# Kernel tuning notes

Hardware: AMD Instinct MI355X
Metric: run time of the kernel (lower is better)

The kernel has to match this reference:

```python
import jax, jax.numpy as jnp
import numpy as np

# Static multi-scale pyramid metadata (spatial_shapes / level_start_index in torch)
SHAPES = [(92, 160), (46, 80), (23, 40), (12, 20)]
B, NQ, C, NH, DH, L, P, DFF = 2, 10000, 256, 8, 32, 4, 4, 1024
S = sum(h * w for h, w in SHAPES)


def layer_norm(x, g, b, eps=1e-5):
    m = x.mean(-1, keepdims=True)
    v = ((x - m) ** 2).mean(-1, keepdims=True)
    return (x - m) * jax.lax.rsqrt(v + eps) * g + b


def ms_deform(value, loc, attn):
    """Multi-scale deformable attention core (grid_sample bilinear, zero padding).
    value: [B,S,NH,DH], loc: [B,NQ,NH,L,P,2] normalized (x,y), attn: [B,NQ,NH,L,P]."""
    out = jnp.zeros((B, NH, NQ, DH), value.dtype)
    start = 0
    for lvl, (Hh, Ww) in enumerate(SHAPES):
        v = value[:, start:start + Hh * Ww].transpose(0, 2, 1, 3)  # [B,NH,HW,DH]
        start += Hh * Ww
        l = loc[:, :, :, lvl].transpose(0, 2, 1, 3, 4)             # [B,NH,NQ,P,2]
        # align_corners=False pixel coords
        x = l[..., 0] * Ww - 0.5
        y = l[..., 1] * Hh - 0.5
        x0 = jnp.floor(x); y0 = jnp.floor(y)
        lx = x - x0; ly = y - y0
        x0i = x0.astype(jnp.int32); y0i = y0.astype(jnp.int32)
        samp = jnp.zeros((B, NH, NQ, P, DH), value.dtype)
        for dx, dy, w in ((0, 0, (1 - lx) * (1 - ly)), (1, 0, lx * (1 - ly)),
                          (0, 1, (1 - lx) * ly), (1, 1, lx * ly)):
            xi = x0i + dx; yi = y0i + dy
            valid = (xi >= 0) & (xi < Ww) & (yi >= 0) & (yi < Hh)
            idx = (jnp.clip(yi, 0, Hh - 1) * Ww + jnp.clip(xi, 0, Ww - 1)).reshape(B, NH, NQ * P)
            g = jnp.take_along_axis(v, jnp.broadcast_to(idx[..., None], (B, NH, NQ * P, DH)), axis=2)
            samp = samp + g.reshape(B, NH, NQ, P, DH) * (w * valid)[..., None]
        out = out + jnp.einsum('bhnpd,bhnp->bhnd', samp, attn[:, :, :, lvl].transpose(0, 2, 1, 3))
    return out.transpose(0, 2, 1, 3).reshape(B, NQ, NH * DH)


def setup_inputs() -> dict:
    ks = jax.random.split(jax.random.key(0), 12)
    sc = C ** -0.5
    return {
        'src': jax.random.normal(ks[0], (B, S, C), jnp.float32),
        'q_feat': jax.random.normal(ks[1], (B, NQ, C), jnp.float32),
        'q_pos': jax.random.normal(ks[2], (B, NQ, C), jnp.float32) * 0.1,
        'q_ref': jax.random.uniform(ks[3], (B, NQ, 2), jnp.float32),
        'valid_ratios': jnp.ones((B, L, 2), jnp.float32),
        'Wv': jax.random.normal(ks[4], (C, C), jnp.float32) * sc,
        'bv': jnp.zeros((C,), jnp.float32),
        'Woff': jax.random.normal(ks[5], (C, NH * L * P * 2), jnp.float32) * 0.01,
        'boff': jax.random.uniform(ks[6], (NH * L * P * 2,), jnp.float32, minval=-0.5, maxval=0.5),
        'Wa': jax.random.normal(ks[7], (C, NH * L * P), jnp.float32) * sc,
        'ba': jnp.zeros((NH * L * P,), jnp.float32),
        'Wo': jax.random.normal(ks[8], (C, C), jnp.float32) * sc,
        'bo': jnp.zeros((C,), jnp.float32),
        'g1': jnp.ones((C,), jnp.float32), 'be1': jnp.zeros((C,), jnp.float32),
        'W1': jax.random.normal(ks[9], (C, DFF), jnp.float32) * sc,
        'bf1': jnp.zeros((DFF,), jnp.float32),
        'W2': jax.random.normal(ks[10], (DFF, C), jnp.float32) * (DFF ** -0.5),
        'bf2': jnp.zeros((C,), jnp.float32),
        'g2': jnp.ones((C,), jnp.float32), 'be2': jnp.zeros((C,), jnp.float32),
    }


def reference(src, q_feat, q_pos, q_ref, valid_ratios, Wv, bv, Woff, boff, Wa, ba,
              Wo, bo, g1, be1, W1, bf1, W2, bf2, g2, be2):
    # reference_points = q_reference_points[:,:,None] * valid_ratios[:,None]
    ref = q_ref[:, :, None, :] * valid_ratios[:, None]          # [B,NQ,L,2]
    # MSDeformAttn
    value = (src @ Wv + bv).reshape(B, S, NH, DH)
    q = q_feat + q_pos
    off = (q @ Woff + boff).reshape(B, NQ, NH, L, P, 2)
    attn = jax.nn.softmax((q @ Wa + ba).reshape(B, NQ, NH, L * P), axis=-1).reshape(B, NQ, NH, L, P)
    normalizer = jnp.array([[w, h] for h, w in SHAPES], src.dtype)  # [L,2] (W,H)
    loc = ref[:, :, None, :, None, :] + off / normalizer[None, None, None, :, None, :]
    a = ms_deform(value, loc, attn) @ Wo + bo
    # residual + LN + FFN (dropout is identity at inference)
    x = layer_norm(q_feat + a, g1, be1)
    ffn = jax.nn.relu(x @ W1 + bf1) @ W2 + bf2
    return layer_norm(x + ffn, g2, be2)
```

## Files before the change

kernel.cpp:

```cpp
#include <hip/hip_runtime.h>
#include <hip/hip_bf16.h>
#include <cstdint>

#define B_   2
#define NQ_  10000
#define C_   256
#define NH_  8
#define DH_  32
#define DFF_ 1024
#define S_   19560
#define MQ_P 20096
#define MV_P 39168

typedef __attribute__((ext_vector_type(8))) short short8;
typedef __attribute__((ext_vector_type(4))) float f32x4;

__device__ __forceinline__ void gload16(const void* g, void* l) {
  __builtin_amdgcn_global_load_lds(
      (const __attribute__((address_space(1))) unsigned int*)g,
      (__attribute__((address_space(3))) unsigned int*)l, 16, 0, 0);
}

__device__ __forceinline__ float bflo(unsigned u) {
  union { unsigned u; float f; } c; c.u = u << 16; return c.f;
}
__device__ __forceinline__ float bfhi(unsigned u) {
  union { unsigned u; float f; } c; c.u = u & 0xffff0000u; return c.f;
}

__global__ __launch_bounds__(256) void conv_weights(
    const float* __restrict__ Wv, const float* __restrict__ Woff,
    const float* __restrict__ Wa, const float* __restrict__ Wo,
    const float* __restrict__ W1, const float* __restrict__ W2,
    __hip_bfloat16* __restrict__ wbase) {
  __shared__ float tile[64][65];
  int blk = blockIdx.x;
  const float* W; __hip_bfloat16* Wt; int K, N;
  if (blk < 16)       { W = Wv;   Wt = wbase + 0;      K = 256;  N = 256; }
  else if (blk < 32)  { W = Woff; Wt = wbase + 65536;  K = 256;  N = 256;  blk -= 16; }
  else if (blk < 40)  { W = Wa;   Wt = wbase + 131072; K = 256;  N = 128;  blk -= 32; }
  else if (blk < 56)  { W = Wo;   Wt = wbase + 163840; K = 256;  N = 256;  blk -= 40; }
  else if (blk < 120) { W = W1;   Wt = wbase + 229376; K = 256;  N = 1024; blk -= 56; }
  else                { W = W2;   Wt = wbase + 491520; K = 1024; N = 256;  blk -= 120; }
  const int ntiles = N >> 6;
  const int kt = blk / ntiles, nt = blk % ntiles;
  const int c = threadIdx.x & 63, r0 = threadIdx.x >> 6;
#pragma unroll
  for (int i = 0; i < 16; ++i) {
    const int r = r0 + i * 4;
    tile[r][c] = W[(long)(kt * 64 + r) * N + nt * 64 + c];
  }
  __syncthreads();
#pragma unroll
  for (int i = 0; i < 16; ++i) {
    const int n = r0 + i * 4;
    Wt[(long)(nt * 64 + n) * K + kt * 64 + c] = __float2bfloat16(tile[c][n]);
  }
}

__global__ __launch_bounds__(256) void prep_q(
    const float* __restrict__ qf, const float* __restrict__ qp,
    __hip_bfloat16* __restrict__ q_bf) {
  long idx = (long)blockIdx.x * 256 + threadIdx.x;
  int row = idx >> 5, c8 = (idx & 31) * 8;
  union { __hip_bfloat16 h[8]; uint4 u; } o;
  if (row < B_ * NQ_) {
    const float4 a0 = *reinterpret_cast<const float4*>(qf + (long)row * 256 + c8);
    const float4 a1 = *reinterpret_cast<const float4*>(qf + (long)row * 256 + c8 + 4);
    const float4 b0 = *reinterpret_cast<const float4*>(qp + (long)row * 256 + c8);
    const float4 b1 = *reinterpret_cast<const float4*>(qp + (long)row * 256 + c8 + 4);
    o.h[0] = __float2bfloat16(a0.x + b0.x); o.h[1] = __float2bfloat16(a0.y + b0.y);
    o.h[2] = __float2bfloat16(a0.z + b0.z); o.h[3] = __float2bfloat16(a0.w + b0.w);
    o.h[4] = __float2bfloat16(a1.x + b1.x); o.h[5] = __float2bfloat16(a1.y + b1.y);
    o.h[6] = __float2bfloat16(a1.z + b1.z); o.h[7] = __float2bfloat16(a1.w + b1.w);
  } else o.u = make_uint4(0, 0, 0, 0);
  *reinterpret_cast<uint4*>(q_bf + (long)row * 256 + c8) = o.u;
}

template <int MODE>
__global__ __launch_bounds__(256) void gemm_bf16(
    const __hip_bfloat16* __restrict__ A, const __hip_bfloat16* __restrict__ Bt,
    const float* __restrict__ bias, const float* __restrict__ bias2, int bsplit,
    void* __restrict__ Cp, int M, int N, int K) {
  __shared__ short smA[64 * 64];
  __shared__ short smB[128 * 64];
  const int tid = threadIdx.x;
  const int lane = tid & 63;
  const int w = tid >> 6;
  const int wr = w >> 1, wc = w & 1;
  const long bm = (long)blockIdx.x * 64;
  const long bn = (long)blockIdx.y * 128;

  f32x4 acc[2][4];
#pragma unroll
  for (int i = 0; i < 2; ++i)
#pragma unroll
    for (int j = 0; j < 4; ++j) acc[i][j] = (f32x4)(0.f);

  const int srow = tid >> 3;
  const int su = (tid & 7) ^ (srow & 7);
  const __hip_bfloat16* Ag = A + (bm + srow) * (long)K + su * 8;
  const __hip_bfloat16* Bg = Bt + (bn + srow) * (long)K + su * 8;
  char* lA = (char*)smA + tid * 16;
  char* lB = (char*)smB + tid * 16;

  for (int k0 = 0; k0 < K; k0 += 64) {
    gload16(Ag,           lA);
    gload16(Ag + 32L * K, lA + 4096);
    gload16(Bg,           lB);
    gload16(Bg + 32L * K, lB + 4096);
    gload16(Bg + 64L * K, lB + 8192);
    gload16(Bg + 96L * K, lB + 12288);
    Ag += 64; Bg += 64;
    __syncthreads();
#pragma unroll
    for (int ks = 0; ks < 2; ++ks) {
      const int u = ks * 4 + (lane >> 4);
      short8 af[2], bf[4];
#pragma unroll
      for (int mi = 0; mi < 2; ++mi) {
        const int r = wr * 32 + (lane & 15) + mi * 16;
        af[mi] = *reinterpret_cast<const short8*>(
            (char*)smA + r * 128 + ((u ^ (r & 7)) * 16));
      }
#pragma unroll
      for (int ni = 0; ni < 4; ++ni) {
        const int r = wc * 64 + (lane & 15) + ni * 16;
        bf[ni] = *reinterpret_cast<const short8*>(
            (char*)smB + r * 128 + ((u ^ (r & 7)) * 16));
      }
#pragma unroll
      for (int mi = 0; mi < 2; ++mi)
#pragma unroll
        for (int ni = 0; ni < 4; ++ni)
          acc[mi][ni] = __builtin_amdgcn_mfma_f32_16x16x32_bf16(af[mi], bf[ni], acc[mi][ni], 0, 0, 0);
    }
    __syncthreads();
  }

  const int crow0 = wr * 32 + ((lane >> 4) << 2);
  const int ccol0 = wc * 64 + (lane & 15);
#pragma unroll
  for (int mi = 0; mi < 2; ++mi) {
#pragma unroll
    for (int ni = 0; ni < 4; ++ni) {
      const int col = bn + ccol0 + ni * 16;
      const float bs = (col < bsplit) ? bias[col] : bias2[col - bsplit];
#pragma unroll
      for (int r = 0; r < 4; ++r) {
        const long row = bm + crow0 + mi * 16 + r;
        float v = acc[mi][ni][r] + bs;
        if (MODE == 0) {
          ((float*)Cp)[row * N + col] = v;
        } else if (MODE == 2) {
          ((__hip_bfloat16*)Cp)[row * N + col] = __float2bfloat16(fmaxf(v, 0.f));
        } else {
          ((__hip_bfloat16*)Cp)[row * N + col] = __float2bfloat16(v);
        }
      }
    }
  }
}

__global__ __launch_bounds__(256) void gemm_val(
    const float* __restrict__ A, const __hip_bfloat16* __restrict__ Bt,
    const float* __restrict__ bias, __hip_bfloat16* __restrict__ Cp, int Mreal) {
  __shared__ short smA[64 * 64];
  __shared__ short smB[256 * 64];
  const int tid = threadIdx.x;
  const int lane = tid & 63;
  const int w = tid >> 6;
  const long bm = (long)blockIdx.x * 64;

  f32x4 acc[4][4];
#pragma unroll
  for (int i = 0; i < 4; ++i)
#pragma unroll
    for (int j = 0; j < 4; ++j) acc[i][j] = (f32x4)(0.f);

  const int ar = tid >> 2;
  const int au = (tid & 3) * 2;
  const bool arow_ok = (bm + ar) < Mreal;
  const float* Afp = A + (bm + ar) * 256L + au * 8;
  char* wA0 = (char*)smA + ar * 128 + ((au ^ (ar & 7)) * 16);
  char* wA1 = (char*)smA + ar * 128 + (((au + 1) ^ (ar & 7)) * 16);

  const int srow = tid >> 3;
  const int su = (tid & 7) ^ (srow & 7);
  const __hip_bfloat16* Bg = Bt + (long)srow * 256 + su * 8;
  char* lB = (char*)smB + tid * 16;

  for (int k0 = 0; k0 < 256; k0 += 64) {
#pragma unroll
    for (int j = 0; j < 8; ++j) gload16(Bg + 32L * j * 256, lB + 4096 * j);
    Bg += 64;
    float4 f0 = make_float4(0.f, 0.f, 0.f, 0.f), f1 = f0, f2 = f0, f3 = f0;
    if (arow_ok) {
      f0 = *reinterpret_cast<const float4*>(Afp + k0);
      f1 = *reinterpret_cast<const float4*>(Afp + k0 + 4);
      f2 = *reinterpret_cast<const float4*>(Afp + k0 + 8);
      f3 = *reinterpret_cast<const float4*>(Afp + k0 + 12);
    }
    union { __hip_bfloat16 h[8]; uint4 u; } c0, c1;
    c0.h[0] = __float2bfloat16(f0.x); c0.h[1] = __float2bfloat16(f0.y);
    c0.h[2] = __float2bfloat16(f0.z); c0.h[3] = __float2bfloat16(f0.w);
    c0.h[4] = __float2bfloat16(f1.x); c0.h[5] = __float2bfloat16(f1.y);
    c0.h[6] = __float2bfloat16(f1.z); c0.h[7] = __float2bfloat16(f1.w);
    c1.h[0] = __float2bfloat16(f2.x); c1.h[1] = __float2bfloat16(f2.y);
    c1.h[2] = __float2bfloat16(f2.z); c1.h[3] = __float2bfloat16(f2.w);
    c1.h[4] = __float2bfloat16(f3.x); c1.h[5] = __float2bfloat16(f3.y);
    c1.h[6] = __float2bfloat16(f3.z); c1.h[7] = __float2bfloat16(f3.w);
    *reinterpret_cast<uint4*>(wA0) = c0.u;
    *reinterpret_cast<uint4*>(wA1) = c1.u;
    __syncthreads();
#pragma unroll
    for (int ks = 0; ks < 2; ++ks) {
      const int u = ks * 4 + (lane >> 4);
      short8 af[4], bf[4];
#pragma unroll
      for (int mi = 0; mi < 4; ++mi) {
        const int r = (lane & 15) + mi * 16;
        af[mi] = *reinterpret_cast<const short8*>(
            (char*)smA + r * 128 + ((u ^ (r & 7)) * 16));
      }
#pragma unroll
      for (int ni = 0; ni < 4; ++ni) {
        const int r = w * 64 + ni * 16 + (lane & 15);
        bf[ni] = *reinterpret_cast<const short8*>(
            (char*)smB + r * 128 + ((u ^ (r & 7)) * 16));
      }
#pragma unroll
      for (int mi = 0; mi < 4; ++mi)
#pragma unroll
        for (int ni = 0; ni < 4; ++ni)
          acc[mi][ni] = __builtin_amdgcn_mfma_f32_16x16x32_bf16(af[mi], bf[ni], acc[mi][ni], 0, 0, 0);
    }
    __syncthreads();
  }

  const int crow0 = (lane >> 4) << 2;
  const int cl = lane & 15;
#pragma unroll
  for (int mi = 0; mi < 4; ++mi) {
#pragma unroll
    for (int ni = 0; ni < 4; ++ni) {
      const int col = w * 64 + ni * 16 + cl;
      const float bs = bias[col];
      const int h = col >> 5, dh = col & 31;
#pragma unroll
      for (int r = 0; r < 4; ++r) {
        const long row = bm + mi * 16 + crow0 + r;
        if (row < Mreal) {
          const int b = (row >= S_) ? 1 : 0;
          const long s = row - (long)b * S_;
          Cp[(((long)(b * 8 + h)) * S_ + s) * 32 + dh] =
              __float2bfloat16(acc[mi][ni][r] + bs);
        }
      }
    }
  }
}

__global__ __launch_bounds__(256) void msdeform_kernel(
    const __hip_bfloat16* __restrict__ value, const __hip_bfloat16* __restrict__ oa,
    const float* __restrict__ q_ref, const float* __restrict__ vr,
    __hip_bfloat16* __restrict__ out) {
  const int t = blockIdx.x * 256 + threadIdx.x;
  const int tid7 = t & 127;
  const int dq = tid7 & 3;
  const int l = (tid7 >> 2) & 3;
  const int h = tid7 >> 4;
  const int bq = __builtin_amdgcn_readfirstlane(t >> 7);
  const int b = (bq >= NQ_) ? 1 : 0;

  const int W  = (l == 0) ? 160 : (l == 1) ? 80 : (l == 2) ? 40 : 20;
  const int H  = (l == 0) ? 92  : (l == 1) ? 46 : (l == 2) ? 23 : 12;
  const int S0 = (l == 0) ? 0 : (l == 1) ? 14720 : (l == 2) ? 18400 : 19320;

  const __hip_bfloat16* oabase = oa + (long)bq * 384;
  const uint2 mu = *reinterpret_cast<const uint2*>(oabase + 256 + h * 16 + l * 4);
  const float l0 = bflo(mu.x), l1 = bfhi(mu.x), l2 = bflo(mu.y), l3 = bfhi(mu.y);
  float mx = fmaxf(fmaxf(l0, l1), fmaxf(l2, l3));
  mx = fmaxf(mx, __shfl_xor(mx, 4, 64));
  mx = fmaxf(mx, __shfl_xor(mx, 8, 64));
  const float e0 = __expf(l0 - mx), e1 = __expf(l1 - mx);
  const float e2 = __expf(l2 - mx), e3 = __expf(l3 - mx);
  float sum = e0 + e1 + e2 + e3;
  sum += __shfl_xor(sum, 4, 64);
  sum += __shfl_xor(sum, 8, 64);
  const float inv = 1.f / sum;
  const float w0 = e0 * inv, w1 = e1 * inv, w2 = e2 * inv, w3 = e3 * inv;

  const uint4 ou = *reinterpret_cast<const uint4*>(oabase + h * 32 + l * 8);

  const float rx = q_ref[(long)bq * 2 + 0];
  const float ry = q_ref[(long)bq * 2 + 1];
  const float2 vv = *reinterpret_cast<const float2*>(vr + (b * 4 + l) * 2);
  const float refxW = rx * vv.x * W - 0.5f;
  const float refyH = ry * vv.y * H - 0.5f;
  const unsigned base32 = (unsigned)(((b * 8 + h) * S_ + S0) * 32 + dq * 8);

  unsigned offs[16]; float wts[16];
#define COORD(s, OX, OY, AW)                                                   \
  {                                                                            \
    const float x = refxW + (OX);                                              \
    const float y = refyH + (OY);                                              \
    const float x0f = floorf(x), y0f = floorf(y);                              \
    const float lx = x - x0f, ly = y - y0f;                                    \
    const int x0 = (int)x0f, y0 = (int)y0f;                                    \
    const int x1 = x0 + 1, y1 = y0 + 1;                                        \
    const float wx0 = ((unsigned)x0 < (unsigned)W) ? (1.f - lx) : 0.f;         \
    const float wx1 = ((unsigned)x1 < (unsigned)W) ? lx : 0.f;                 \
    const float wy0 = ((unsigned)y0 < (unsigned)H) ? (1.f - ly) : 0.f;         \
    const float wy1 = ((unsigned)y1 < (unsigned)H) ? ly : 0.f;                 \
    const int x0c = min(max(x0, 0), W - 1);                                    \
    const int x1c = min(max(x1, 0), W - 1);                                    \
    const int y0c = min(max(y0, 0), H - 1);                                    \
    const int y1c = min(max(y1, 0), H - 1);                                    \
    const unsigned r0o = base32 + (unsigned)(y0c * W) * 32;                    \
    const unsigned r1o = base32 + (unsigned)(y1c * W) * 32;                    \
    offs[4 * (s) + 0] = r0o + (unsigned)x0c * 32;                              \
    offs[4 * (s) + 1] = r0o + (unsigned)x1c * 32;                              \
    offs[4 * (s) + 2] = r1o + (unsigned)x0c * 32;                              \
    offs[4 * (s) + 3] = r1o + (unsigned)x1c * 32;                              \
    wts[4 * (s) + 0] = (AW) * wx0 * wy0;                                       \
    wts[4 * (s) + 1] = (AW) * wx1 * wy0;                                       \
    wts[4 * (s) + 2] = (AW) * wx0 * wy1;                                       \
    wts[4 * (s) + 3] = (AW) * wx1 * wy1;                                       \
  }
  COORD(0, bflo(ou.x), bfhi(ou.x), w0)
  COORD(1, bflo(ou.y), bfhi(ou.y), w1)
  COORD(2, bflo(ou.z), bfhi(ou.z), w2)
  COORD(3, bflo(ou.w), bfhi(ou.w), w3)
#undef COORD

  uint4 d[16];
#pragma unroll
  for (int j = 0; j < 16; ++j)
    d[j] = *reinterpret_cast<const uint4*>(value + offs[j]);
  __builtin_amdgcn_sched_barrier(0);

  float acc[8] = {};
#pragma unroll
  for (int j = 0; j < 16; ++j) {
    const float ww = wts[j];
    acc[0] += ww * bflo(d[j].x); acc[1] += ww * bfhi(d[j].x);
    acc[2] += ww * bflo(d[j].y); acc[3] += ww * bfhi(d[j].y);
    acc[4] += ww * bflo(d[j].z); acc[5] += ww * bfhi(d[j].z);
    acc[6] += ww * bflo(d[j].w); acc[7] += ww * bfhi(d[j].w);
  }

#pragma unroll
  for (int j = 0; j < 8; ++j) acc[j] += __shfl_xor(acc[j], 4, 64);
#pragma unroll
  for (int j = 0; j < 8; ++j) acc[j] += __shfl_xor(acc[j], 8, 64);

  if (l == 0) {
    union { __hip_bfloat16 hh[8]; uint4 u; } o0;
#pragma unroll
    for (int j = 0; j < 8; ++j) o0.hh[j] = __float2bfloat16(acc[j]);
    *reinterpret_cast<uint4*>(out + (long)bq * 256 + h * 32 + dq * 8) = o0.u;
  }
}

__global__ __launch_bounds__(256) void add_ln_kernel(
    const float* __restrict__ res, const float* __restrict__ xin,
    const float* __restrict__ gamma, const float* __restrict__ beta,
    float* __restrict__ out, __hip_bfloat16* __restrict__ out_bf, int nrows) {
  int row = blockIdx.x * 4 + (threadIdx.x >> 6);
  int lane = threadIdx.x & 63;
  if (row >= nrows) return;
  const float4 r4 = *reinterpret_cast<const float4*>(res + (long)row * 256 + lane * 4);
  const float4 x4 = *reinterpret_cast<const float4*>(xin + (long)row * 256 + lane * 4);
  float tv[4] = {r4.x + x4.x, r4.y + x4.y, r4.z + x4.z, r4.w + x4.w};
  float s = tv[0] + tv[1] + tv[2] + tv[3];
#pragma unroll
  for (int o = 32; o > 0; o >>= 1) s += __shfl_xor(s, o, 64);
  float mean = s * (1.f / 256.f);
  float vs = 0.f;
#pragma unroll
  for (int j = 0; j < 4; ++j) { float dd = tv[j] - mean; vs += dd * dd; }
#pragma unroll
  for (int o = 32; o > 0; o >>= 1) vs += __shfl_xor(vs, o, 64);
  float inv = rsqrtf(vs * (1.f / 256.f) + 1e-5f);
  const float4 g = *reinterpret_cast<const float4*>(gamma + lane * 4);
  const float4 be = *reinterpret_cast<const float4*>(beta + lane * 4);
  float4 o4;
  o4.x = (tv[0] - mean) * inv * g.x + be.x;
  o4.y = (tv[1] - mean) * inv * g.y + be.y;
  o4.z = (tv[2] - mean) * inv * g.z + be.z;
  o4.w = (tv[3] - mean) * inv * g.w + be.w;
  *reinterpret_cast<float4*>(out + (long)row * 256 + lane * 4) = o4;
  if (out_bf) {
    union { __hip_bfloat16 h[4]; uint2 u; } p;
    p.h[0] = __float2bfloat16(o4.x); p.h[1] = __float2bfloat16(o4.y);
    p.h[2] = __float2bfloat16(o4.z); p.h[3] = __float2bfloat16(o4.w);
    *reinterpret_cast<uint2*>(out_bf + (long)row * 256 + lane * 4) = p.u;
  }
}

extern "C" void kernel_launch(void* const* d_in, const int* in_sizes, int n_in,
                              void* d_out, int out_size, void* d_ws, size_t ws_size,
                              hipStream_t stream) {
  const float* src    = (const float*)d_in[0];
  const float* q_feat = (const float*)d_in[1];
  const float* q_pos  = (const float*)d_in[2];
  const float* q_ref  = (const float*)d_in[3];
  const float* vr     = (const float*)d_in[4];
  const float* Wv     = (const float*)d_in[5];
  const float* bv     = (const float*)d_in[6];
  const float* Woff   = (const float*)d_in[7];
  const float* boff   = (const float*)d_in[8];
  const float* Wa     = (const float*)d_in[9];
  const float* ba     = (const float*)d_in[10];
  const float* Wo     = (const float*)d_in[11];
  const float* bo     = (const float*)d_in[12];
  const float* g1     = (const float*)d_in[13];
  const float* be1    = (const float*)d_in[14];
  const float* W1     = (const float*)d_in[15];
  const float* bf1    = (const float*)d_in[16];
  const float* W2     = (const float*)d_in[17];
  const float* bf2    = (const float*)d_in[18];
  const float* g2     = (const float*)d_in[19];
  const float* be2    = (const float*)d_in[20];

  char* ws = (char*)d_ws;
  __hip_bfloat16* val_bf = (__hip_bfloat16*)(ws + 0);
  __hip_bfloat16* q_bf   = (__hip_bfloat16*)(ws + 20029440);
  float*          a_f    = (float*)(ws + 0);
  __hip_bfloat16* h1_bf  = (__hip_bfloat16*)(ws + 0);
  __hip_bfloat16* oa_bf  = (__hip_bfloat16*)(ws + 41156608);
  float*          f2_f   = (float*)(ws + 41156608);
  __hip_bfloat16* ms_bf  = (__hip_bfloat16*)(ws + 61734912);
  float*          x_f    = (float*)(ws + 72024064);
  __hip_bfloat16* x_bf   = (__hip_bfloat16*)(ws + 92602368);
  __hip_bfloat16* wts    = (__hip_bfloat16*)(ws + 102891520);
  float* outp = (float*)d_out;

  const int Mq = B_ * NQ_;
  const int Mv = B_ * S_;
  const int BIG = 1 << 30;

  conv_weights<<<184, 256, 0, stream>>>(Wv, Woff, Wa, Wo, W1, W2, wts);
  prep_q<<<MQ_P * 32 / 256, 256, 0, stream>>>(q_feat, q_pos, q_bf);
  gemm_val<<<MV_P / 64, 256, 0, stream>>>(src, wts + 0, bv, val_bf, Mv);
  gemm_bf16<4><<<dim3(MQ_P / 64, 3), 256, 0, stream>>>(q_bf, wts + 65536, boff, ba, 256, oa_bf, MQ_P, 384, 256);
  msdeform_kernel<<<(Mq * 128) / 256, 256, 0, stream>>>(val_bf, oa_bf, q_ref, vr, ms_bf);
  gemm_bf16<0><<<dim3(MQ_P / 64, 2), 256, 0, stream>>>(ms_bf, wts + 163840, bo, bo, BIG, a_f, MQ_P, 256, 256);
  add_ln_kernel<<<(Mq + 3) / 4, 256, 0, stream>>>(q_feat, a_f, g1, be1, x_f, x_bf, Mq);
  gemm_bf16<2><<<dim3(MQ_P / 64, 8), 256, 0, stream>>>(x_bf, wts + 229376, bf1, bf1, BIG, h1_bf, MQ_P, 1024, 256);
  gemm_bf16<0><<<dim3(MQ_P / 64, 2), 256, 0, stream>>>(h1_bf, wts + 491520, bf2, bf2, BIG, f2_f, MQ_P, 256, 1024);
  add_ln_kernel<<<(Mq + 3) / 4, 256, 0, stream>>>(x_f, f2_f, g2, be2, outp, nullptr, Mq);
}
```

Measured before the change: 167.9 us.

## Store intermediate activations in bf16, merge prep kernels, pack deform accumulation

```diff
diff --git a/kernel.cpp b/kernel.cpp
--- a/kernel.cpp
+++ b/kernel.cpp
@@ -14,6 +14,7 @@
 
 typedef __attribute__((ext_vector_type(8))) short short8;
 typedef __attribute__((ext_vector_type(4))) float f32x4;
+typedef __attribute__((ext_vector_type(2))) float f32x2;
 
 __device__ __forceinline__ void gload16(const void* g, void* l) {
   __builtin_amdgcn_global_load_lds(
@@ -28,53 +29,53 @@
   union { unsigned u; float f; } c; c.u = u & 0xffff0000u; return c.f;
 }
 
-__global__ __launch_bounds__(256) void conv_weights(
+__global__ __launch_bounds__(256) void prep_all(
     const float* __restrict__ Wv, const float* __restrict__ Woff,
     const float* __restrict__ Wa, const float* __restrict__ Wo,
     const float* __restrict__ W1, const float* __restrict__ W2,
-    __hip_bfloat16* __restrict__ wbase) {
-  __shared__ float tile[64][65];
-  int blk = blockIdx.x;
-  const float* W; __hip_bfloat16* Wt; int K, N;
-  if (blk < 16)       { W = Wv;   Wt = wbase + 0;      K = 256;  N = 256; }
-  else if (blk < 32)  { W = Woff; Wt = wbase + 65536;  K = 256;  N = 256;  blk -= 16; }
-  else if (blk < 40)  { W = Wa;   Wt = wbase + 131072; K = 256;  N = 128;  blk -= 32; }
-  else if (blk < 56)  { W = Wo;   Wt = wbase + 163840; K = 256;  N = 256;  blk -= 40; }
-  else if (blk < 120) { W = W1;   Wt = wbase + 229376; K = 256;  N = 1024; blk -= 56; }
-  else                { W = W2;   Wt = wbase + 491520; K = 1024; N = 256;  blk -= 120; }
-  const int ntiles = N >> 6;
-  const int kt = blk / ntiles, nt = blk % ntiles;
-  const int c = threadIdx.x & 63, r0 = threadIdx.x >> 6;
-#pragma unroll
-  for (int i = 0; i < 16; ++i) {
-    const int r = r0 + i * 4;
-    tile[r][c] = W[(long)(kt * 64 + r) * N + nt * 64 + c];
-  }
-  __syncthreads();
-#pragma unroll
-  for (int i = 0; i < 16; ++i) {
-    const int n = r0 + i * 4;
-    Wt[(long)(nt * 64 + n) * K + kt * 64 + c] = __float2bfloat16(tile[c][n]);
-  }
-}
-
-__global__ __launch_bounds__(256) void prep_q(
+    __hip_bfloat16* __restrict__ wbase,
     const float* __restrict__ qf, const float* __restrict__ qp,
     __hip_bfloat16* __restrict__ q_bf) {
-  long idx = (long)blockIdx.x * 256 + threadIdx.x;
-  int row = idx >> 5, c8 = (idx & 31) * 8;
-  union { __hip_bfloat16 h[8]; uint4 u; } o;
-  if (row < B_ * NQ_) {
-    const float4 a0 = *reinterpret_cast<const float4*>(qf + (long)row * 256 + c8);
-    const float4 a1 = *reinterpret_cast<const float4*>(qf + (long)row * 256 + c8 + 4);
-    const float4 b0 = *reinterpret_cast<const float4*>(qp + (long)row * 256 + c8);
-    const float4 b1 = *reinterpret_cast<const float4*>(qp + (long)row * 256 + c8 + 4);
-    o.h[0] = __float2bfloat16(a0.x + b0.x); o.h[1] = __float2bfloat16(a0.y + b0.y);
-    o.h[2] = __float2bfloat16(a0.z + b0.z); o.h[3] = __float2bfloat16(a0.w + b0.w);
-    o.h[4] = __float2bfloat16(a1.x + b1.x); o.h[5] = __float2bfloat16(a1.y + b1.y);
-    o.h[6] = __float2bfloat16(a1.z + b1.z); o.h[7] = __float2bfloat16(a1.w + b1.w);
-  } else o.u = make_uint4(0, 0, 0, 0);
-  *reinterpret_cast<uint4*>(q_bf + (long)row * 256 + c8) = o.u;
+  __shared__ float tile[64][65];
+  if (blockIdx.x < 184) {
+    int blk = blockIdx.x;
+    const float* W; __hip_bfloat16* Wt; int K, N;
+    if (blk < 16)       { W = Wv;   Wt = wbase + 0;      K = 256;  N = 256; }
+    else if (blk < 32)  { W = Woff; Wt = wbase + 65536;  K = 256;  N = 256;  blk -= 16; }
+    else if (blk < 40)  { W = Wa;   Wt = wbase + 131072; K = 256;  N = 128;  blk -= 32; }
+    else if (blk < 56)  { W = Wo;   Wt = wbase + 163840; K = 256;  N = 256;  blk -= 40; }
+    else if (blk < 120) { W = W1;   Wt = wbase + 229376; K = 256;  N = 1024; blk -= 56; }
+    else                { W = W2;   Wt = wbase + 491520; K = 1024; N = 256;  blk -= 120; }
+    const int ntiles = N >> 6;
+    const int kt = blk / ntiles, nt = blk % ntiles;
+    const int c = threadIdx.x & 63, r0 = threadIdx.x >> 6;
+#pragma unroll
+    for (int i = 0; i < 16; ++i) {
+      const int r = r0 + i * 4;
+      tile[r][c] = W[(long)(kt * 64 + r) * N + nt * 64 + c];
+    }
+    __syncthreads();
+#pragma unroll
+    for (int i = 0; i < 16; ++i) {
+      const int n = r0 + i * 4;
+      Wt[(long)(nt * 64 + n) * K + kt * 64 + c] = __float2bfloat16(tile[c][n]);
+    }
+  } else {
+    long idx = (long)(blockIdx.x - 184) * 256 + threadIdx.x;
+    int row = idx >> 5, c8 = (idx & 31) * 8;
+    union { __hip_bfloat16 h[8]; uint4 u; } o;
+    if (row < B_ * NQ_) {
+      const float4 a0 = *reinterpret_cast<const float4*>(qf + (long)row * 256 + c8);
+      const float4 a1 = *reinterpret_cast<const float4*>(qf + (long)row * 256 + c8 + 4);
+      const float4 b0 = *reinterpret_cast<const float4*>(qp + (long)row * 256 + c8);
+      const float4 b1 = *reinterpret_cast<const float4*>(qp + (long)row * 256 + c8 + 4);
+      o.h[0] = __float2bfloat16(a0.x + b0.x); o.h[1] = __float2bfloat16(a0.y + b0.y);
+      o.h[2] = __float2bfloat16(a0.z + b0.z); o.h[3] = __float2bfloat16(a0.w + b0.w);
+      o.h[4] = __float2bfloat16(a1.x + b1.x); o.h[5] = __float2bfloat16(a1.y + b1.y);
+      o.h[6] = __float2bfloat16(a1.z + b1.z); o.h[7] = __float2bfloat16(a1.w + b1.w);
+    } else o.u = make_uint4(0, 0, 0, 0);
+    *reinterpret_cast<uint4*>(q_bf + (long)row * 256 + c8) = o.u;
+  }
 }
 
 template <int MODE>
@@ -150,9 +151,7 @@
       for (int r = 0; r < 4; ++r) {
         const long row = bm + crow0 + mi * 16 + r;
         float v = acc[mi][ni][r] + bs;
-        if (MODE == 0) {
-          ((float*)Cp)[row * N + col] = v;
-        } else if (MODE == 2) {
+        if (MODE == 2) {
           ((__hip_bfloat16*)Cp)[row * N + col] = __float2bfloat16(fmaxf(v, 0.f));
         } else {
           ((__hip_bfloat16*)Cp)[row * N + col] = __float2bfloat16(v);
@@ -340,39 +339,57 @@
     d[j] = *reinterpret_cast<const uint4*>(value + offs[j]);
   __builtin_amdgcn_sched_barrier(0);
 
-  float acc[8] = {};
+  f32x2 acc2[4];
+#pragma unroll
+  for (int i = 0; i < 4; ++i) acc2[i] = (f32x2)(0.f);
 #pragma unroll
   for (int j = 0; j < 16; ++j) {
-    const float ww = wts[j];
-    acc[0] += ww * bflo(d[j].x); acc[1] += ww * bfhi(d[j].x);
-    acc[2] += ww * bflo(d[j].y); acc[3] += ww * bfhi(d[j].y);
-    acc[4] += ww * bflo(d[j].z); acc[5] += ww * bfhi(d[j].z);
-    acc[6] += ww * bflo(d[j].w); acc[7] += ww * bfhi(d[j].w);
-  }
-
-#pragma unroll
-  for (int j = 0; j < 8; ++j) acc[j] += __shfl_xor(acc[j], 4, 64);
-#pragma unroll
-  for (int j = 0; j < 8; ++j) acc[j] += __shfl_xor(acc[j], 8, 64);
+    const f32x2 ww2 = (f32x2)(wts[j]);
+    f32x2 v0, v1, v2, v3;
+    v0.x = bflo(d[j].x); v0.y = bfhi(d[j].x);
+    v1.x = bflo(d[j].y); v1.y = bfhi(d[j].y);
+    v2.x = bflo(d[j].z); v2.y = bfhi(d[j].z);
+    v3.x = bflo(d[j].w); v3.y = bfhi(d[j].w);
+    acc2[0] += ww2 * v0;
+    acc2[1] += ww2 * v1;
+    acc2[2] += ww2 * v2;
+    acc2[3] += ww2 * v3;
+  }
+
+  float accf[8] = {acc2[0].x, acc2[0].y, acc2[1].x, acc2[1].y,
+                   acc2[2].x, acc2[2].y, acc2[3].x, acc2[3].y};
+#pragma unroll
+  for (int j = 0; j < 8; ++j) accf[j] += __shfl_xor(accf[j], 4, 64);
+#pragma unroll
+  for (int j = 0; j < 8; ++j) accf[j] += __shfl_xor(accf[j], 8, 64);
 
   if (l == 0) {
     union { __hip_bfloat16 hh[8]; uint4 u; } o0;
 #pragma unroll
-    for (int j = 0; j < 8; ++j) o0.hh[j] = __float2bfloat16(acc[j]);
+    for (int j = 0; j < 8; ++j) o0.hh[j] = __float2bfloat16(accf[j]);
     *reinterpret_cast<uint4*>(out + (long)bq * 256 + h * 32 + dq * 8) = o0.u;
   }
 }
 
-__global__ __launch_bounds__(256) void add_ln_kernel(
-    const float* __restrict__ res, const float* __restrict__ xin,
+template <bool RES_F32, bool OUT_F32>
+__global__ __launch_bounds__(256) void add_ln2(
+    const void* __restrict__ resv, const __hip_bfloat16* __restrict__ xin,
     const float* __restrict__ gamma, const float* __restrict__ beta,
-    float* __restrict__ out, __hip_bfloat16* __restrict__ out_bf, int nrows) {
+    float* __restrict__ outF, __hip_bfloat16* __restrict__ outB, int nrows) {
   int row = blockIdx.x * 4 + (threadIdx.x >> 6);
   int lane = threadIdx.x & 63;
   if (row >= nrows) return;
-  const float4 r4 = *reinterpret_cast<const float4*>(res + (long)row * 256 + lane * 4);
-  const float4 x4 = *reinterpret_cast<const float4*>(xin + (long)row * 256 + lane * 4);
-  float tv[4] = {r4.x + x4.x, r4.y + x4.y, r4.z + x4.z, r4.w + x4.w};
+  float rv[4];
+  if (RES_F32) {
+    const float4 r4 = *reinterpret_cast<const float4*>((const float*)resv + (long)row * 256 + lane * 4);
+    rv[0] = r4.x; rv[1] = r4.y; rv[2] = r4.z; rv[3] = r4.w;
+  } else {
+    const uint2 r2 = *reinterpret_cast<const uint2*>((const __hip_bfloat16*)resv + (long)row * 256 + lane * 4);
+    rv[0] = bflo(r2.x); rv[1] = bfhi(r2.x); rv[2] = bflo(r2.y); rv[3] = bfhi(r2.y);
+  }
+  const uint2 x2 = *reinterpret_cast<const uint2*>(xin + (long)row * 256 + lane * 4);
+  float tv[4] = {rv[0] + bflo(x2.x), rv[1] + bfhi(x2.x),
+                 rv[2] + bflo(x2.y), rv[3] + bfhi(x2.y)};
   float s = tv[0] + tv[1] + tv[2] + tv[3];
 #pragma unroll
   for (int o = 32; o > 0; o >>= 1) s += __shfl_xor(s, o, 64);
@@ -385,17 +402,19 @@
   float inv = rsqrtf(vs * (1.f / 256.f) + 1e-5f);
   const float4 g = *reinterpret_cast<const float4*>(gamma + lane * 4);
   const float4 be = *reinterpret_cast<const float4*>(beta + lane * 4);
-  float4 o4;
-  o4.x = (tv[0] - mean) * inv * g.x + be.x;
-  o4.y = (tv[1] - mean) * inv * g.y + be.y;
-  o4.z = (tv[2] - mean) * inv * g.z + be.z;
-  o4.w = (tv[3] - mean) * inv * g.w + be.w;
-  *reinterpret_cast<float4*>(out + (long)row * 256 + lane * 4) = o4;
-  if (out_bf) {
+  float o4[4];
+  o4[0] = (tv[0] - mean) * inv * g.x + be.x;
+  o4[1] = (tv[1] - mean) * inv * g.y + be.y;
+  o4[2] = (tv[2] - mean) * inv * g.z + be.z;
+  o4[3] = (tv[3] - mean) * inv * g.w + be.w;
+  if (OUT_F32) {
+    float4 of = {o4[0], o4[1], o4[2], o4[3]};
+    *reinterpret_cast<float4*>(outF + (long)row * 256 + lane * 4) = of;
+  } else {
     union { __hip_bfloat16 h[4]; uint2 u; } p;
-    p.h[0] = __float2bfloat16(o4.x); p.h[1] = __float2bfloat16(o4.y);
-    p.h[2] = __float2bfloat16(o4.z); p.h[3] = __float2bfloat16(o4.w);
-    *reinterpret_cast<uint2*>(out_bf + (long)row * 256 + lane * 4) = p.u;
+    p.h[0] = __float2bfloat16(o4[0]); p.h[1] = __float2bfloat16(o4[1]);
+    p.h[2] = __float2bfloat16(o4[2]); p.h[3] = __float2bfloat16(o4[3]);
+    *reinterpret_cast<uint2*>(outB + (long)row * 256 + lane * 4) = p.u;
   }
 }
 
@@ -427,13 +446,12 @@
   char* ws = (char*)d_ws;
   __hip_bfloat16* val_bf = (__hip_bfloat16*)(ws + 0);
   __hip_bfloat16* q_bf   = (__hip_bfloat16*)(ws + 20029440);
-  float*          a_f    = (float*)(ws + 0);
+  __hip_bfloat16* a_bf   = (__hip_bfloat16*)(ws + 0);
   __hip_bfloat16* h1_bf  = (__hip_bfloat16*)(ws + 0);
   __hip_bfloat16* oa_bf  = (__hip_bfloat16*)(ws + 41156608);
-  float*          f2_f   = (float*)(ws + 41156608);
+  __hip_bfloat16* f2_bf  = (__hip_bfloat16*)(ws + 41156608);
   __hip_bfloat16* ms_bf  = (__hip_bfloat16*)(ws + 61734912);
-  float*          x_f    = (float*)(ws + 72024064);
-  __hip_bfloat16* x_bf   = (__hip_bfloat16*)(ws + 92602368);
+  __hip_bfloat16* x_bf   = (__hip_bfloat16*)(ws + 72024064);
   __hip_bfloat16* wts    = (__hip_bfloat16*)(ws + 102891520);
   float* outp = (float*)d_out;
 
@@ -441,14 +459,14 @@
   const int Mv = B_ * S_;
   const int BIG = 1 << 30;
 
-  conv_weights<<<184, 256, 0, stream>>>(Wv, Woff, Wa, Wo, W1, W2, wts);
-  prep_q<<<MQ_P * 32 / 256, 256, 0, stream>>>(q_feat, q_pos, q_bf);
+  prep_all<<<184 + MQ_P * 32 / 256, 256, 0, stream>>>(Wv, Woff, Wa, Wo, W1, W2, wts,
+                                                      q_feat, q_pos, q_bf);
   gemm_val<<<MV_P / 64, 256, 0, stream>>>(src, wts + 0, bv, val_bf, Mv);
   gemm_bf16<4><<<dim3(MQ_P / 64, 3), 256, 0, stream>>>(q_bf, wts + 65536, boff, ba, 256, oa_bf, MQ_P, 384, 256);
   msdeform_kernel<<<(Mq * 128) / 256, 256, 0, stream>>>(val_bf, oa_bf, q_ref, vr, ms_bf);
-  gemm_bf16<0><<<dim3(MQ_P / 64, 2), 256, 0, stream>>>(ms_bf, wts + 163840, bo, bo, BIG, a_f, MQ_P, 256, 256);
-  add_ln_kernel<<<(Mq + 3) / 4, 256, 0, stream>>>(q_feat, a_f, g1, be1, x_f, x_bf, Mq);
+  gemm_bf16<4><<<dim3(MQ_P / 64, 2), 256, 0, stream>>>(ms_bf, wts + 163840, bo, bo, BIG, a_bf, MQ_P, 256, 256);
+  add_ln2<true, false><<<(Mq + 3) / 4, 256, 0, stream>>>(q_feat, a_bf, g1, be1, nullptr, x_bf, Mq);
   gemm_bf16<2><<<dim3(MQ_P / 64, 8), 256, 0, stream>>>(x_bf, wts + 229376, bf1, bf1, BIG, h1_bf, MQ_P, 1024, 256);
-  gemm_bf16<0><<<dim3(MQ_P / 64, 2), 256, 0, stream>>>(h1_bf, wts + 491520, bf2, bf2, BIG, f2_f, MQ_P, 256, 1024);
-  add_ln_kernel<<<(Mq + 3) / 4, 256, 0, stream>>>(x_f, f2_f, g2, be2, outp, nullptr, Mq);
-}
+  gemm_bf16<4><<<dim3(MQ_P / 64, 2), 256, 0, stream>>>(h1_bf, wts + 491520, bf2, bf2, BIG, f2_bf, MQ_P, 256, 1024);
+  add_ln2<false, true><<<(Mq + 3) / 4, 256, 0, stream>>>(x_bf, f2_bf, g2, be2, outp, nullptr, Mq);
+}
```

After: 154.6 us. -7.9%, faster.
